# Kernel optimization log

Measured on AMD Instinct MI355X. Metric: run time of the kernel, lower is better.

Reference implementation:

```python
import jax, jax.numpy as jnp
import numpy as np

N = 50000      # nodes
E = 500000     # edges
G = 8          # graphs in batch
H = 64         # latent width (message_passer out_channels)
FIN = 5        # raw node feature dim
MDIM = 3       # mask dim (last col = BC flag)
EF = 3         # edge feature dim
OUT = 4        # output dim
REPEATS = 4    # message passing repeats


def _mlp(h, w1, b1, w2, b2):
    return jnp.dot(jax.nn.relu(jnp.dot(h, w1) + b1), w2) + b2


def _seg_mean(v, idx, n):
    s = jax.ops.segment_sum(v, idx, num_segments=n)
    c = jax.ops.segment_sum(jnp.ones((v.shape[0], 1), v.dtype), idx, num_segments=n)
    return s / jnp.maximum(c, 1.0)


def _lin(k, fi, fo):
    return (jax.random.normal(k, (fi, fo), jnp.float32) / np.sqrt(fi),
            jnp.zeros((fo,), jnp.float32))


def setup_inputs() -> dict:
    key = jax.random.key(0)
    ks = jax.random.split(key, 16)
    x = jax.random.normal(ks[0], (N, FIN), jnp.float32)
    x_mask = jax.random.uniform(ks[1], (N, MDIM), jnp.float32)
    x_mask = x_mask.at[:, -1].set((x_mask[:, -1] > 0.9).astype(jnp.float32))
    edge_index = jax.random.randint(ks[2], (2, E), 0, N, jnp.int32)
    edge_attr = jax.random.normal(ks[3], (E, EF), jnp.float32)
    pos = jax.random.uniform(ks[4], (N, 2), jnp.float32)
    batch = jnp.sort(jax.random.randint(ks[5], (N,), 0, G, jnp.int32))
    enc_w1, enc_b1 = _lin(ks[6], FIN + MDIM, H)
    enc_w2, enc_b2 = _lin(ks[7], H, H)
    msg_w1, msg_b1 = _lin(ks[8], 2 * H + EF, H)
    msg_w2, msg_b2 = _lin(ks[9], H, H)
    upd_w1, upd_b1 = _lin(ks[10], 4 * H, H)
    upd_w2, upd_b2 = _lin(ks[11], H, H)
    dec_w1, dec_b1 = _lin(ks[12], H, H)
    dec_w2, dec_b2 = _lin(ks[13], H, OUT)
    return dict(x=x, x_mask=x_mask, edge_index=edge_index, edge_attr=edge_attr,
                pos=pos, batch=batch,
                enc_w1=enc_w1, enc_b1=enc_b1, enc_w2=enc_w2, enc_b2=enc_b2,
                msg_w1=msg_w1, msg_b1=msg_b1, msg_w2=msg_w2, msg_b2=msg_b2,
                upd_w1=upd_w1, upd_b1=upd_b1, upd_w2=upd_w2, upd_b2=upd_b2,
                dec_w1=dec_w1, dec_b1=dec_b1, dec_w2=dec_w2, dec_b2=dec_b2)


def reference(x, x_mask, edge_index, edge_attr, pos, batch,
              enc_w1, enc_b1, enc_w2, enc_b2,
              msg_w1, msg_b1, msg_w2, msg_b2,
              upd_w1, upd_b1, upd_w2, upd_b2,
              dec_w1, dec_b1, dec_w2, dec_b2):
    # x = concat([x, x_mask]); BC_idxs = x_mask[:, -1]
    bc = x_mask[:, -1:]                                   # [N,1] 0/1 BC flag
    h = _mlp(jnp.concatenate([x, x_mask], axis=1), enc_w1, enc_b1, enc_w2, enc_b2)
    # x_BC = scatter-mean of encoded BC nodes per graph (mask-weighted segment mean)
    bc_sum = jax.ops.segment_sum(h * bc, batch, num_segments=G)
    bc_cnt = jax.ops.segment_sum(bc, batch, num_segments=G)
    x_BC = bc_sum / jnp.maximum(bc_cnt, 1.0)              # [G,H]
    x_graph = _seg_mean(h, batch, G)                      # global_mean_pool [G,H]
    src, dst = edge_index[0], edge_index[1]
    for _ in range(REPEATS):
        # message: MLP over [x_src, x_dst, edge_attr], scatter-mean to dst
        m = _mlp(jnp.concatenate([h[src], h[dst], edge_attr], axis=1),
                 msg_w1, msg_b1, msg_w2, msg_b2)          # [E,H]
        agg = _seg_mean(m, dst, N)                        # [N,H]
        # node update conditioned on global and BC context, residual
        h = h + _mlp(jnp.concatenate([h, agg, x_graph[batch], x_BC[batch]], axis=1),
                     upd_w1, upd_b1, upd_w2, upd_b2)
        x_graph = _seg_mean(h, batch, G)                  # refreshed each repeat
    return _mlp(h, dec_w1, dec_b1, dec_w2, dec_b2)        # [N,OUT]
```

## Files before the change

kernel.cpp:

```cpp
#include <hip/hip_runtime.h>
#include <hip/hip_bf16.h>

#define NN 50000
#define EE 500000
#define GG 8
#define NB 196

#define SCALE_A 65536.0f
#define INV_SCALE_A (1.0f/65536.0f)
#define SCALE_G 16777216.0f
#define INV_SCALE_G (1.0f/16777216.0f)

using short8 = __attribute__((ext_vector_type(8))) short;
using f32x16 = __attribute__((ext_vector_type(16))) float;

__device__ __forceinline__ float4 ld4(const float* p){ return *reinterpret_cast<const float4*>(p); }

__device__ __forceinline__ short f2b(float f){
  union { __hip_bfloat16 b; short s; } u;
  u.b = __float2bfloat16(f);
  return u.s;
}

__global__ __launch_bounds__(256) void k_count(const int* __restrict__ dst, int* __restrict__ cnt){
  int e = blockIdx.x*256 + threadIdx.x;
  if (e < EE) atomicAdd(&cnt[dst[e]], 1);
}

__global__ __launch_bounds__(256) void k_scanA(const int* __restrict__ cnt, int* __restrict__ bsum){
  __shared__ int s[256];
  int t = threadIdx.x;
  int i = blockIdx.x*256 + t;
  s[t] = (i < NN) ? cnt[i] : 0;
  __syncthreads();
  for (int o=128;o>0;o>>=1){ if (t<o) s[t]+=s[t+o]; __syncthreads(); }
  if (t==0) bsum[blockIdx.x] = s[0];
}

__global__ __launch_bounds__(256) void k_scanB(const int* __restrict__ bsum, int* __restrict__ boff){
  __shared__ int s[256];
  int t = threadIdx.x;
  s[t] = (t < NB) ? bsum[t] : 0;
  __syncthreads();
  for (int o=1;o<256;o<<=1){
    int u = (t>=o) ? s[t-o] : 0;
    __syncthreads();
    s[t] += u;
    __syncthreads();
  }
  if (t < NB) boff[t] = (t==0) ? 0 : s[t-1];
}

__global__ __launch_bounds__(256) void k_scanC_prep(const int* __restrict__ cnt, const int* __restrict__ boff,
                                               int* __restrict__ offs,
                                               float* __restrict__ inv, const int* __restrict__ batch,
                                               const float* __restrict__ xm,
                                               float* __restrict__ ncnt, float* __restrict__ bccnt){
  __shared__ int s[256];
  __shared__ float lc[GG], lb[GG];
  int t = threadIdx.x;
  int i = blockIdx.x*256 + t;
  if (t < GG){ lc[t]=0.f; lb[t]=0.f; }
  int v = (i < NN) ? cnt[i] : 0;
  s[t] = v;
  __syncthreads();
  for (int o=1;o<256;o<<=1){
    int u = (t>=o) ? s[t-o] : 0;
    __syncthreads();
    s[t] += u;
    __syncthreads();
  }
  if (i < NN){
    offs[i] = boff[blockIdx.x] + s[t] - v;
    inv[i] = 1.0f / fmaxf((float)v, 1.0f);
    int g = batch[i];
    atomicAdd(&lc[g], 1.0f);
    atomicAdd(&lb[g], xm[i*3+2]);
  }
  __syncthreads();
  if (t < GG){ atomicAdd(&ncnt[t], lc[t]); atomicAdd(&bccnt[t], lb[t]); }
}

__global__ __launch_bounds__(256) void k_prep(const int* __restrict__ cnt, float* __restrict__ inv,
                       const int* __restrict__ batch, const float* __restrict__ xm,
                       float* __restrict__ ncnt, float* __restrict__ bccnt){
  __shared__ float lc[GG], lb[GG];
  int t = threadIdx.x;
  if (t < GG){ lc[t]=0.f; lb[t]=0.f; }
  __syncthreads();
  int i = blockIdx.x*256 + t;
  if (i < NN){
    inv[i] = 1.0f / fmaxf((float)cnt[i], 1.0f);
    int g = batch[i];
    atomicAdd(&lc[g], 1.0f);
    atomicAdd(&lb[g], xm[i*3+2]);
  }
  __syncthreads();
  if (t < GG){ atomicAdd(&ncnt[t], lc[t]); atomicAdd(&bccnt[t], lb[t]); }
}

__global__ __launch_bounds__(256) void k_scat1(const int* __restrict__ dst, int* __restrict__ offs,
                                               int* __restrict__ perm){
  int e = blockIdx.x*256 + threadIdx.x;
  if (e >= EE) return;
  int d = dst[e];
  int pos = atomicAdd(&offs[d], 1);
  perm[pos] = e;
}

__global__ __launch_bounds__(256) void k_scat2(const int* __restrict__ perm,
                                               const int* __restrict__ src, const int* __restrict__ dst,
                                               const float* __restrict__ ea,
                                               int* __restrict__ srcs_s, int* __restrict__ dsts_s,
                                               short* __restrict__ ea16){
  int i = blockIdx.x*256 + threadIdx.x;
  if (i >= EE) return;
  int e = perm[i];
  srcs_s[i] = src[e];
  dsts_s[i] = dst[e];
  int lo = ((int)(unsigned short)f2b(ea[(size_t)e*3+0])) |
           (((int)(unsigned short)f2b(ea[(size_t)e*3+1])) << 16);
  int hi = ((int)(unsigned short)f2b(ea[(size_t)e*3+2]));
  int2 v; v.x = lo; v.y = hi;
  *(int2*)(ea16 + (size_t)i*4) = v;
}

__device__ __forceinline__ void packone(const float* __restrict__ w, int Kreal, int idx, short* __restrict__ out){
  int k = idx >> 6, n = idx & 63;
  float v = (k < Kreal) ? w[k*64 + n] : 0.f;
  int ks = k >> 4, kl = k & 15;
  int lane = (n & 31) + 32*(kl >> 3);
  int e = kl & 7;
  out[(ks*2 + (n>>5))*512 + lane*8 + e] = f2b(v);
}

__global__ __launch_bounds__(256) void k_wpack(
    const float* __restrict__ mw1, const float* __restrict__ mw2,
    const float* __restrict__ uw1, const float* __restrict__ uw2,
    short* __restrict__ mw1p, short* __restrict__ mw2p,
    short* __restrict__ uw1p, short* __restrict__ uw2p){
  int gid = blockIdx.x*256 + threadIdx.x;
  int stride = gridDim.x*256;
  for (int i=gid; i<144*64; i+=stride) packone(mw1, 131, i, mw1p);
  for (int i=gid; i<64*64;  i+=stride) packone(mw2, 64,  i, mw2p);
  for (int i=gid; i<256*64; i+=stride) packone(uw1, 256, i, uw1p);
  for (int i=gid; i<64*64;  i+=stride) packone(uw2, 64,  i, uw2p);
}

__global__ __launch_bounds__(256) void k_enc(
    const float* __restrict__ x, const float* __restrict__ xm,
    const float* __restrict__ w1, const float* __restrict__ b1,
    const float* __restrict__ w2, const float* __restrict__ b2,
    float* __restrict__ h, short* __restrict__ h16){
  __shared__ float w1s[8*64];
  __shared__ float w2s[64*64];
  __shared__ float b1s[64], b2s[64];
  __shared__ float ols[4][64][17];
  int t = threadIdx.x;
  for (int i=t;i<8*64;i+=256) w1s[i]=w1[i];
  for (int i=t;i<64*64;i+=256) w2s[i]=w2[i];
  if (t<64){ b1s[t]=b1[t]; b2s[t]=b2[t]; }
  __syncthreads();
  const int w = t >> 6, lane = t & 63;
  const int base_w = blockIdx.x*256 + w*64;
  const int n = base_w + lane;
  const int nc = (n < NN) ? n : (NN-1);
  float in[8];
  #pragma unroll
  for (int k=0;k<5;k++) in[k] = x[nc*5+k];
  #pragma unroll
  for (int k=0;k<3;k++) in[5+k] = xm[nc*3+k];
  float hid[64];
  #pragma unroll
  for (int o=0;o<64;o++){
    float a = b1s[o];
    #pragma unroll
    for (int k=0;k<8;k++) a += in[k]*w1s[k*64+o];
    hid[o] = fmaxf(a, 0.f);
  }
  for (int c=0;c<4;c++){
    float a[16];
    #pragma unroll
    for (int j=0;j<16;j++) a[j] = b2s[c*16+j];
    for (int k=0;k<64;k++){
      float hv = hid[k];
      #pragma unroll
      for (int j=0;j<16;j++) a[j] += hv * w2s[k*64 + c*16 + j];
    }
    #pragma unroll
    for (int j=0;j<16;j++) ols[w][lane][j] = a[j];
    __syncthreads();
    #pragma unroll
    for (int p=0;p<4;p++){
      int nd = p*16 + (lane>>2);
      int jj = lane & 3;
      int ng = base_w + nd;
      if (ng < NN){
        float4 v = make_float4(ols[w][nd][jj*4+0], ols[w][nd][jj*4+1],
                               ols[w][nd][jj*4+2], ols[w][nd][jj*4+3]);
        *(float4*)(h + (size_t)ng*64 + c*16 + jj*4) = v;
      }
    }
    #pragma unroll
    for (int p=0;p<2;p++){
      int nd = p*32 + (lane>>1);
      int jj = (lane & 1)*8;
      int ng = base_w + nd;
      if (ng < NN){
        short8 s;
        #pragma unroll
        for (int q=0;q<8;q++) s[q] = f2b(ols[w][nd][jj+q]);
        *(short8*)(h16 + (size_t)ng*64 + c*16 + jj) = s;
      }
    }
    __syncthreads();
  }
}

__global__ __launch_bounds__(256) void k_gred(
    const float* __restrict__ h, const int* __restrict__ batch,
    const float* __restrict__ xm,
    unsigned long long* __restrict__ xg_sum, unsigned long long* __restrict__ xbc_sum, int withBC){
  __shared__ float ls[4][GG][64];
  __shared__ float lb[4][GG][64];
  int t = threadIdx.x;
  int d = t & 63, grp = t >> 6;
  for (int g=0; g<GG; g++){ ls[grp][g][d]=0.f; lb[grp][g][d]=0.f; }
  __syncthreads();
  for (int i = blockIdx.x*4 + grp; i < NN; i += gridDim.x*4){
    int g = batch[i];
    float v = h[(size_t)i*64 + d];
    ls[grp][g][d] += v;
    if (withBC) lb[grp][g][d] += v * xm[i*3+2];
  }
  __syncthreads();
  if (t < 64){
    for (int g=0; g<GG; g++){
      float s = ls[0][g][d]+ls[1][g][d]+ls[2][g][d]+ls[3][g][d];
      atomicAdd(&xg_sum[g*64+d], (unsigned long long)(long long)llrintf(s*SCALE_G));
    }
  } else if (withBC && t < 128){
    int dd = t & 63;
    for (int g=0; g<GG; g++){
      float s = lb[0][g][dd]+lb[1][g][dd]+lb[2][g][dd]+lb[3][g][dd];
      atomicAdd(&xbc_sum[g*64+dd], (unsigned long long)(long long)llrintf(s*SCALE_G));
    }
  }
}

__global__ void k_gfin(unsigned long long* __restrict__ xg_sum, const unsigned long long* __restrict__ xbc_sum,
                       const float* __restrict__ ncnt, const float* __restrict__ bccnt,
                       short* __restrict__ xg16, short* __restrict__ xbc16, int withBC){
  int t = threadIdx.x;
  int g = t >> 6;
  float sg = (float)(long long)xg_sum[t] * INV_SCALE_G;
  xg16[t] = f2b(sg / fmaxf(ncnt[g], 1.f));
  xg_sum[t] = 0;
  if (withBC){
    float sb = (float)(long long)xbc_sum[t] * INV_SCALE_G;
    xbc16[t] = f2b(sb / fmaxf(bccnt[g], 1.f));
  }
}

__global__ __launch_bounds__(256) void k_msg_s(
    const short* __restrict__ h16,
    const int* __restrict__ srcs_s, const int* __restrict__ dsts_s,
    const short* __restrict__ ea16,
    const short* __restrict__ w1p, const float* __restrict__ b1,
    const short* __restrict__ w2p, const float* __restrict__ b2,
    int* __restrict__ agg){
  __shared__ int buf[4][2304];
  const int t = threadIdx.x;
  const int w = t >> 6, lane = t & 63;
  const int r = lane & 31, khalf = lane >> 5;
  const int base = blockIdx.x*256 + w*64;

  const int slot = base + lane;
  const int dl = (slot < EE) ? dsts_s[slot] : -1;

  const int eA = base + r, eB = base + 32 + r;
  const bool vA = eA < EE, vB = eB < EE;
  const int sA = vA ? srcs_s[eA] : 0;
  const int sB = vB ? srcs_s[eB] : 0;
  int dA = __shfl(dl, r);        if (dA < 0) dA = 0;
  int dB = __shfl(dl, 32 + r);   if (dB < 0) dB = 0;

  float b1v0 = b1[r], b1v1 = b1[32 + r];
  f32x16 acc00, acc01, acc10, acc11;
  #pragma unroll
  for (int j=0;j<16;j++){ acc00[j]=b1v0; acc01[j]=b1v1; acc10[j]=b1v0; acc11[j]=b1v1; }

  const short8* w1f = (const short8*)w1p;
  #pragma unroll
  for (int ks=0; ks<9; ks++){
    short8 a0, a1;
    if (ks < 8){
      long offA, offB;
      if (ks < 4){
        offA = (long)sA*64 + ks*16 + khalf*8;
        offB = (long)sB*64 + ks*16 + khalf*8;
      } else {
        offA = (long)dA*64 + (ks-4)*16 + khalf*8;
        offB = (long)dB*64 + (ks-4)*16 + khalf*8;
      }
      a0 = *(const short8*)(h16 + offA);
      a1 = *(const short8*)(h16 + offB);
    } else {
      #pragma unroll
      for (int j=0;j<8;j++){ a0[j]=0; a1[j]=0; }
      if (khalf == 0){
        if (vA){
          int2 v = *(const int2*)(ea16 + (size_t)eA*4);
          a0[0]=(short)v.x; a0[1]=(short)(v.x>>16); a0[2]=(short)v.y; a0[3]=(short)(v.y>>16);
        }
        if (vB){
          int2 v = *(const int2*)(ea16 + (size_t)eB*4);
          a1[0]=(short)v.x; a1[1]=(short)(v.x>>16); a1[2]=(short)v.y; a1[3]=(short)(v.y>>16);
        }
      }
    }
    short8 bf0 = w1f[(ks*2+0)*64 + lane];
    short8 bf1 = w1f[(ks*2+1)*64 + lane];
    acc00 = __builtin_amdgcn_mfma_f32_32x32x16_bf16(a0, bf0, acc00, 0, 0, 0);
    acc01 = __builtin_amdgcn_mfma_f32_32x32x16_bf16(a0, bf1, acc01, 0, 0, 0);
    acc10 = __builtin_amdgcn_mfma_f32_32x32x16_bf16(a1, bf0, acc10, 0, 0, 0);
    acc11 = __builtin_amdgcn_mfma_f32_32x32x16_bf16(a1, bf1, acc11, 0, 0, 0);
  }

  short* hw = (short*)&buf[w][0];
  #pragma unroll
  for (int reg=0; reg<16; reg++){
    int row = (reg&3) + 8*(reg>>2) + 4*khalf;
    hw[(row     )*72 + r     ] = f2b(fmaxf(acc00[reg], 0.f));
    hw[(row     )*72 + 32 + r] = f2b(fmaxf(acc01[reg], 0.f));
    hw[(row + 32)*72 + r     ] = f2b(fmaxf(acc10[reg], 0.f));
    hw[(row + 32)*72 + 32 + r] = f2b(fmaxf(acc11[reg], 0.f));
  }

  float b2v0 = b2[r], b2v1 = b2[32 + r];
  f32x16 c00, c01, c10, c11;
  #pragma unroll
  for (int j=0;j<16;j++){ c00[j]=b2v0; c01[j]=b2v1; c10[j]=b2v0; c11[j]=b2v1; }

  const short8* w2f = (const short8*)w2p;
  #pragma unroll
  for (int ks=0; ks<4; ks++){
    short8 a0 = *(const short8*)(hw + (r     )*72 + ks*16 + khalf*8);
    short8 a1 = *(const short8*)(hw + (32 + r)*72 + ks*16 + khalf*8);
    short8 bf0 = w2f[(ks*2+0)*64 + lane];
    short8 bf1 = w2f[(ks*2+1)*64 + lane];
    c00 = __builtin_amdgcn_mfma_f32_32x32x16_bf16(a0, bf0, c00, 0, 0, 0);
    c01 = __builtin_amdgcn_mfma_f32_32x32x16_bf16(a0, bf1, c01, 0, 0, 0);
    c10 = __builtin_amdgcn_mfma_f32_32x32x16_bf16(a1, bf0, c10, 0, 0, 0);
    c11 = __builtin_amdgcn_mfma_f32_32x32x16_bf16(a1, bf1, c11, 0, 0, 0);
  }

  int* mb = &buf[w][0];

  #pragma unroll
  for (int reg=0; reg<16; reg++){
    int row = (reg&3) + 8*(reg>>2) + 4*khalf;
    mb[row*65 + r     ] = __float2int_rn(c00[reg]*SCALE_A);
    mb[row*65 + 32 + r] = __float2int_rn(c01[reg]*SCALE_A);
  }
  {
    int cur = 0;
    while (cur < 32){
      int d = __shfl(dl, cur);
      unsigned long long diff = __ballot(dl != d);
      unsigned low = (unsigned)diff;
      unsigned rest = low & (0xFFFFFFFEu << cur);
      int end = rest ? (__ffs(rest) - 1) : 32;
      if (d >= 0){
        int s = 0;
        for (int rr=cur; rr<end; rr++) s += mb[rr*65 + lane];
        atomicAdd(&agg[(size_t)d*64 + lane], s);
      }
      cur = end;
    }
  }

  #pragma unroll
  for (int reg=0; reg<16; reg++){
    int row = (reg&3) + 8*(reg>>2) + 4*khalf;
    mb[row*65 + r     ] = __float2int_rn(c10[reg]*SCALE_A);
    mb[row*65 + 32 + r] = __float2int_rn(c11[reg]*SCALE_A);
  }
  {
    int cur = 0;
    while (cur < 32){
      int d = __shfl(dl, 32 + cur);
      unsigned long long diff = __ballot(dl != d);
      unsigned hi = (unsigned)(diff >> 32);
      unsigned rest = hi & (0xFFFFFFFEu << cur);
      int end = rest ? (__ffs(rest) - 1) : 32;
      if (d >= 0){
        int s = 0;
        for (int rr=cur; rr<end; rr++) s += mb[rr*65 + lane];
        atomicAdd(&agg[(size_t)d*64 + lane], s);
      }
      cur = end;
    }
  }
}

__global__ __launch_bounds__(256) void k_msg_atomic(
    const short* __restrict__ h16, const int* __restrict__ src, const int* __restrict__ dst,
    const float* __restrict__ ea,
    const short* __restrict__ w1p, const float* __restrict__ b1,
    const short* __restrict__ w2p, const float* __restrict__ b2,
    int* __restrict__ agg){
  __shared__ short hidT[4][64*72];
  const int t = threadIdx.x;
  const int w = t >> 6, lane = t & 63;
  const int r = lane & 31, khalf = lane >> 5;
  const int base = blockIdx.x*256 + w*64;
  const int eA = base + r, eB = base + 32 + r;
  const bool vA = eA < EE, vB = eB < EE;
  const int sA = vA ? src[eA] : 0, dA_ = vA ? dst[eA] : 0;
  const int sB = vB ? src[eB] : 0, dB_ = vB ? dst[eB] : 0;

  float b1v0 = b1[r], b1v1 = b1[32 + r];
  f32x16 acc00, acc01, acc10, acc11;
  #pragma unroll
  for (int j=0;j<16;j++){ acc00[j]=b1v0; acc01[j]=b1v1; acc10[j]=b1v0; acc11[j]=b1v1; }

  const short8* w1f = (const short8*)w1p;
  #pragma unroll
  for (int ks=0; ks<9; ks++){
    short8 a0, a1;
    if (ks < 8){
      long offA, offB;
      if (ks < 4){
        offA = (long)sA*64 + ks*16 + khalf*8;
        offB = (long)sB*64 + ks*16 + khalf*8;
      } else {
        offA = (long)dA_*64 + (ks-4)*16 + khalf*8;
        offB = (long)dB_*64 + (ks-4)*16 + khalf*8;
      }
      a0 = *(const short8*)(h16 + offA);
      a1 = *(const short8*)(h16 + offB);
    } else {
      #pragma unroll
      for (int j=0;j<8;j++){ a0[j]=0; a1[j]=0; }
      if (khalf == 0){
        if (vA){ a0[0]=f2b(ea[3*eA]); a0[1]=f2b(ea[3*eA+1]); a0[2]=f2b(ea[3*eA+2]); }
        if (vB){ a1[0]=f2b(ea[3*eB]); a1[1]=f2b(ea[3*eB+1]); a1[2]=f2b(ea[3*eB+2]); }
      }
    }
    short8 bf0 = w1f[(ks*2+0)*64 + lane];
    short8 bf1 = w1f[(ks*2+1)*64 + lane];
    acc00 = __builtin_amdgcn_mfma_f32_32x32x16_bf16(a0, bf0, acc00, 0, 0, 0);
    acc01 = __builtin_amdgcn_mfma_f32_32x32x16_bf16(a0, bf1, acc01, 0, 0, 0);
    acc10 = __builtin_amdgcn_mfma_f32_32x32x16_bf16(a1, bf0, acc10, 0, 0, 0);
    acc11 = __builtin_amdgcn_mfma_f32_32x32x16_bf16(a1, bf1, acc11, 0, 0, 0);
  }

  short* hw = &hidT[w][0];
  #pragma unroll
  for (int reg=0; reg<16; reg++){
    int row = (reg&3) + 8*(reg>>2) + 4*khalf;
    hw[(row     )*72 + r     ] = f2b(fmaxf(acc00[reg], 0.f));
    hw[(row     )*72 + 32 + r] = f2b(fmaxf(acc01[reg], 0.f));
    hw[(row + 32)*72 + r     ] = f2b(fmaxf(acc10[reg], 0.f));
    hw[(row + 32)*72 + 32 + r] = f2b(fmaxf(acc11[reg], 0.f));
  }

  float b2v0 = b2[r], b2v1 = b2[32 + r];
  f32x16 c00, c01, c10, c11;
  #pragma unroll
  for (int j=0;j<16;j++){ c00[j]=b2v0; c01[j]=b2v1; c10[j]=b2v0; c11[j]=b2v1; }

  const short8* w2f = (const short8*)w2p;
  #pragma unroll
  for (int ks=0; ks<4; ks++){
    short8 a0 = *(const short8*)(hw + (r     )*72 + ks*16 + khalf*8);
    short8 a1 = *(const short8*)(hw + (32 + r)*72 + ks*16 + khalf*8);
    short8 bf0 = w2f[(ks*2+0)*64 + lane];
    short8 bf1 = w2f[(ks*2+1)*64 + lane];
    c00 = __builtin_amdgcn_mfma_f32_32x32x16_bf16(a0, bf0, c00, 0, 0, 0);
    c01 = __builtin_amdgcn_mfma_f32_32x32x16_bf16(a0, bf1, c01, 0, 0, 0);
    c10 = __builtin_amdgcn_mfma_f32_32x32x16_bf16(a1, bf0, c10, 0, 0, 0);
    c11 = __builtin_amdgcn_mfma_f32_32x32x16_bf16(a1, bf1, c11, 0, 0, 0);
  }

  #pragma unroll
  for (int reg=0; reg<16; reg++){
    int row = (reg&3) + 8*(reg>>2) + 4*khalf;
    int e0r = base + row;
    int e1r = base + 32 + row;
    int d0 = __shfl(dA_, row);
    int d1 = __shfl(dB_, row);
    if (e0r < EE){
      atomicAdd(&agg[(size_t)d0*64 + r     ], __float2int_rn(c00[reg]*SCALE_A));
      atomicAdd(&agg[(size_t)d0*64 + 32 + r], __float2int_rn(c01[reg]*SCALE_A));
    }
    if (e1r < EE){
      atomicAdd(&agg[(size_t)d1*64 + r     ], __float2int_rn(c10[reg]*SCALE_A));
      atomicAdd(&agg[(size_t)d1*64 + 32 + r], __float2int_rn(c11[reg]*SCALE_A));
    }
  }
}

__global__ __launch_bounds__(256) void k_upd(
    float* __restrict__ h32, short* __restrict__ h16,
    int* __restrict__ agg, const float* __restrict__ inv,
    const int* __restrict__ batch,
    const short* __restrict__ xg16, const short* __restrict__ xbc16,
    const short* __restrict__ w1p, const float* __restrict__ b1,
    const short* __restrict__ w2p, const float* __restrict__ b2,
    unsigned long long* __restrict__ xg_sum, int withG){
  __shared__ short hidT[4][32*72];
  __shared__ unsigned long long gs[GG*64];
  const int t = threadIdx.x;
  for (int i=t; i<GG*64; i+=256) gs[i]=0;
  __syncthreads();

  const int w = t >> 6, lane = t & 63;
  const int r = lane & 31, khalf = lane >> 5;
  const int n0 = blockIdx.x*128 + w*32;
  const int n = n0 + r;
  const int nc = (n < NN) ? n : (NN-1);
  const int g = batch[nc];
  const float sc = inv[nc] * INV_SCALE_A;

  float b1v0 = b1[r], b1v1 = b1[32 + r];
  f32x16 a0acc, a1acc;
  #pragma unroll
  for (int j=0;j<16;j++){ a0acc[j]=b1v0; a1acc[j]=b1v1; }

  const short8* w1f = (const short8*)w1p;
  #pragma unroll
  for (int ks=0; ks<16; ks++){
    short8 a;
    int so = (ks & 3)*16 + khalf*8;
    if (ks < 4){
      a = *(const short8*)(h16 + (long)nc*64 + so);
    } else if (ks < 8){
      int4 i0 = *(const int4*)(agg + (long)nc*64 + so);
      int4 i1 = *(const int4*)(agg + (long)nc*64 + so + 4);
      if (n < NN){
        *(int4*)(agg + (long)nc*64 + so)     = make_int4(0,0,0,0);
        *(int4*)(agg + (long)nc*64 + so + 4) = make_int4(0,0,0,0);
      }
      a[0]=f2b((float)i0.x*sc); a[1]=f2b((float)i0.y*sc); a[2]=f2b((float)i0.z*sc); a[3]=f2b((float)i0.w*sc);
      a[4]=f2b((float)i1.x*sc); a[5]=f2b((float)i1.y*sc); a[6]=f2b((float)i1.z*sc); a[7]=f2b((float)i1.w*sc);
    } else if (ks < 12){
      a = *(const short8*)(xg16 + g*64 + so);
    } else {
      a = *(const short8*)(xbc16 + g*64 + so);
    }
    short8 bf0 = w1f[(ks*2+0)*64 + lane];
    short8 bf1 = w1f[(ks*2+1)*64 + lane];
    a0acc = __builtin_amdgcn_mfma_f32_32x32x16_bf16(a, bf0, a0acc, 0, 0, 0);
    a1acc = __builtin_amdgcn_mfma_f32_32x32x16_bf16(a, bf1, a1acc, 0, 0, 0);
  }

  short* hw = &hidT[w][0];
  #pragma unroll
  for (int reg=0; reg<16; reg++){
    int row = (reg&3) + 8*(reg>>2) + 4*khalf;
    hw[row*72 + r     ] = f2b(fmaxf(a0acc[reg], 0.f));
    hw[row*72 + 32 + r] = f2b(fmaxf(a1acc[reg], 0.f));
  }

  float b2v0 = b2[r], b2v1 = b2[32 + r];
  f32x16 c0, c1;
  #pragma unroll
  for (int j=0;j<16;j++){ c0[j]=b2v0; c1[j]=b2v1; }

  const short8* w2f = (const short8*)w2p;
  #pragma unroll
  for (int ks=0; ks<4; ks++){
    short8 a = *(const short8*)(hw + r*72 + ks*16 + khalf*8);
    short8 bf0 = w2f[(ks*2+0)*64 + lane];
    short8 bf1 = w2f[(ks*2+1)*64 + lane];
    c0 = __builtin_amdgcn_mfma_f32_32x32x16_bf16(a, bf0, c0, 0, 0, 0);
    c1 = __builtin_amdgcn_mfma_f32_32x32x16_bf16(a, bf1, c1, 0, 0, 0);
  }

  const bool doG = (withG != 0);
  const int g0 = __shfl(g, 0), g31 = __shfl(g, 31);
  const bool uni = (g0 == g31);
  long long s0 = 0, s1 = 0;
  #pragma unroll
  for (int reg=0; reg<16; reg++){
    int row = (reg&3) + 8*(reg>>2) + 4*khalf;
    int gg = __shfl(g, row);
    int nn = n0 + row;
    if (nn < NN){
      size_t i0 = (size_t)nn*64 + r;
      float v0 = h32[i0] + c0[reg];
      float v1 = h32[i0+32] + c1[reg];
      h32[i0] = v0;    h16[i0] = f2b(v0);
      h32[i0+32] = v1; h16[i0+32] = f2b(v1);
      if (doG){
        long long q0 = llrintf(v0*SCALE_G), q1 = llrintf(v1*SCALE_G);
        if (uni){ s0 += q0; s1 += q1; }
        else {
          atomicAdd(&gs[gg*64 + r     ], (unsigned long long)q0);
          atomicAdd(&gs[gg*64 + 32 + r], (unsigned long long)q1);
        }
      }
    }
  }
  if (doG && uni && (s0|s1)){
    atomicAdd(&gs[g0*64 + r     ], (unsigned long long)s0);
    atomicAdd(&gs[g0*64 + 32 + r], (unsigned long long)s1);
  }
  __syncthreads();
  if (doG){
    for (int i=t; i<GG*64; i+=256){
      unsigned long long v = gs[i];
      if (v) atomicAdd(&xg_sum[i], v);
    }
  }
}

__global__ __launch_bounds__(256) void k_dec(
    const float* __restrict__ h,
    const float* __restrict__ w1, const float* __restrict__ b1,
    const float* __restrict__ w2, const float* __restrict__ b2,
    float* __restrict__ out){
  __shared__ float w1s[64*64];
  __shared__ float w2s[64*4];
  __shared__ float b1s[64], b2s[4];
  int t=threadIdx.x;
  for (int i=t;i<64*64;i+=256) w1s[i]=w1[i];
  for (int i=t;i<256;i+=256) w2s[i]=w2[i];
  if (t<64) b1s[t]=b1[t];
  if (t<4) b2s[t]=b2[t];
  __syncthreads();
  int n = blockIdx.x*256+t;
  if (n>=NN) return;
  float xr[64];
  #pragma unroll
  for (int k=0;k<64;k++) xr[k] = h[(size_t)n*64+k];
  float a0=b2s[0],a1=b2s[1],a2=b2s[2],a3=b2s[3];
  for (int o=0;o<64;o++){
    float a=b1s[o];
    #pragma unroll
    for (int k=0;k<64;k++) a += xr[k]*w1s[k*64+o];
    a = fmaxf(a,0.f);
    a0 += a*w2s[o*4+0]; a1 += a*w2s[o*4+1]; a2 += a*w2s[o*4+2]; a3 += a*w2s[o*4+3];
  }
  out[(size_t)n*4+0]=a0; out[(size_t)n*4+1]=a1; out[(size_t)n*4+2]=a2; out[(size_t)n*4+3]=a3;
}

extern "C" void kernel_launch(void* const* d_in, const int* in_sizes, int n_in,
                              void* d_out, int out_size, void* d_ws, size_t ws_size,
                              hipStream_t stream){
  const float* x   = (const float*)d_in[0];
  const float* xm  = (const float*)d_in[1];
  const int*   ei  = (const int*)d_in[2];
  const float* ea  = (const float*)d_in[3];
  const int* batch = (const int*)d_in[5];
  const float* enc_w1=(const float*)d_in[6],  *enc_b1=(const float*)d_in[7];
  const float* enc_w2=(const float*)d_in[8],  *enc_b2=(const float*)d_in[9];
  const float* msg_w1=(const float*)d_in[10], *msg_b1=(const float*)d_in[11];
  const float* msg_w2=(const float*)d_in[12], *msg_b2=(const float*)d_in[13];
  const float* upd_w1=(const float*)d_in[14], *upd_b1=(const float*)d_in[15];
  const float* upd_w2=(const float*)d_in[16], *upd_b2=(const float*)d_in[17];
  const float* dec_w1=(const float*)d_in[18], *dec_b1=(const float*)d_in[19];
  const float* dec_w2=(const float*)d_in[20], *dec_b2=(const float*)d_in[21];
  const int* srcp = ei;
  const int* dstp = ei + EE;

  char* ws = (char*)d_ws;
  float* h32     = (float*)(ws + 0);
  int*   agg     = (int*)  (ws + 12800000);
  short* h16     = (short*)(ws + 25600000);
  float* inv     = (float*)(ws + 32000000);
  int*   cnt     = (int*)  (ws + 32200000);
  unsigned long long* xg_sum  = (unsigned long long*)(ws + 32400000);
  unsigned long long* xbc_sum = (unsigned long long*)(ws + 32404096);
  float* ncnt    = (float*)(ws + 32408192);
  float* bccnt   = (float*)(ws + 32408224);
  short* xg16    = (short*)(ws + 32408256);
  short* xbc16   = (short*)(ws + 32409280);
  short* mw1p    = (short*)(ws + 32410304);
  short* mw2p    = (short*)(ws + 32428736);
  short* uw1p    = (short*)(ws + 32436928);
  short* uw2p    = (short*)(ws + 32469696);
  int*   offs    = (int*)  (ws + 32477888);
  int*   srcs_s  = (int*)  (ws + 32677888);
  int*   dsts_s  = (int*)  (ws + 34678784);
  short* ea16s   = (short*)(ws + 36679680);
  int*   bsum    = (int*)  (ws + 40681472);
  int*   boff    = (int*)  (ws + 40682272);
  int*   perm    = (int*)  (ws + 40683072);
  const size_t WS_NEED_SORT = 42683968;
  const int useSort = (ws_size >= WS_NEED_SORT) ? 1 : 0;

  hipMemsetAsync(ws + 32200000, 0, 208256, stream);
  hipMemsetAsync(agg, 0, 12800000, stream);
  k_wpack<<<34, 256, 0, stream>>>(msg_w1, msg_w2, upd_w1, upd_w2, mw1p, mw2p, uw1p, uw2p);
  k_count<<<(EE+255)/256, 256, 0, stream>>>(dstp, cnt);
  if (useSort){
    k_scanA<<<NB, 256, 0, stream>>>(cnt, bsum);
    k_scanB<<<1, 256, 0, stream>>>(bsum, boff);
    k_scanC_prep<<<NB, 256, 0, stream>>>(cnt, boff, offs, inv, batch, xm, ncnt, bccnt);
    k_scat1<<<(EE+255)/256, 256, 0, stream>>>(dstp, offs, perm);
    k_scat2<<<(EE+255)/256, 256, 0, stream>>>(perm, srcp, dstp, ea, srcs_s, dsts_s, ea16s);
  } else {
    k_prep<<<(NN+255)/256, 256, 0, stream>>>(cnt, inv, batch, xm, ncnt, bccnt);
  }
  k_enc<<<(NN+255)/256, 256, 0, stream>>>(x, xm, enc_w1, enc_b1, enc_w2, enc_b2, h32, h16);
  k_gred<<<512, 256, 0, stream>>>(h32, batch, xm, xg_sum, xbc_sum, 1);
  k_gfin<<<1, 512, 0, stream>>>(xg_sum, xbc_sum, ncnt, bccnt, xg16, xbc16, 1);

  for (int rp=0; rp<4; rp++){
    if (useSort){
      k_msg_s<<<(EE+255)/256, 256, 0, stream>>>(h16, srcs_s, dsts_s, ea16s, mw1p, msg_b1, mw2p, msg_b2, agg);
    } else {
      k_msg_atomic<<<(EE+255)/256, 256, 0, stream>>>(h16, srcp, dstp, ea, mw1p, msg_b1, mw2p, msg_b2, agg);
    }
    int withG = (rp < 3) ? 1 : 0;
    k_upd<<<(NN+127)/128, 256, 0, stream>>>(h32, h16, agg, inv, batch, xg16, xbc16, uw1p, upd_b1, uw2p, upd_b2, xg_sum, withG);
    if (withG) k_gfin<<<1, 512, 0, stream>>>(xg_sum, xbc_sum, ncnt, bccnt, xg16, xbc16, 0);
  }
  k_dec<<<(NN+255)/256, 256, 0, stream>>>(h32, dec_w1, dec_b1, dec_w2, dec_b2, (float*)d_out);
}
```

Baseline: 412.2 us.

## Halve edges per wave in sorted message kernel and vectorize decoder loads

The sorted-edge message kernel now gives each wave 32 edges instead of 64. It keeps two accumulator tiles instead of four, preloads all nine A fragments up front, and halves the shared-memory buffer by switching it to short. The segmented scatter reduction now runs in two 16-row passes and clamps each segment end to the pass boundary. The aim is lower register and LDS pressure for higher occupancy and better latency hiding of the gathers, at the cost of twice as many blocks, reloading the weight fragments per wave, and possibly more atomics at segment boundaries. The decoder also switches its row loads to float4.

```diff
diff --git a/kernel.cpp b/kernel.cpp
--- a/kernel.cpp
+++ b/kernel.cpp
@@ -269,134 +269,92 @@
     const short* __restrict__ w1p, const float* __restrict__ b1,
     const short* __restrict__ w2p, const float* __restrict__ b2,
     int* __restrict__ agg){
-  __shared__ int buf[4][2304];
+  __shared__ short hid[4][2304];
   const int t = threadIdx.x;
   const int w = t >> 6, lane = t & 63;
   const int r = lane & 31, khalf = lane >> 5;
-  const int base = blockIdx.x*256 + w*64;
-
-  const int slot = base + lane;
-  const int dl = (slot < EE) ? dsts_s[slot] : -1;
-
-  const int eA = base + r, eB = base + 32 + r;
-  const bool vA = eA < EE, vB = eB < EE;
-  const int sA = vA ? srcs_s[eA] : 0;
-  const int sB = vB ? srcs_s[eB] : 0;
-  int dA = __shfl(dl, r);        if (dA < 0) dA = 0;
-  int dB = __shfl(dl, 32 + r);   if (dB < 0) dB = 0;
+  const int base = blockIdx.x*128 + w*32;
+  const int e = base + r;
+  const bool ve = e < EE;
+  const int dl = ve ? dsts_s[e] : -1;
+  const int sA = ve ? srcs_s[e] : 0;
+  const int dA = (dl < 0) ? 0 : dl;
+
+  short8 a[9];
+  #pragma unroll
+  for (int ks=0;ks<4;ks++) a[ks]   = *(const short8*)(h16 + (long)sA*64 + ks*16 + khalf*8);
+  #pragma unroll
+  for (int ks=0;ks<4;ks++) a[4+ks] = *(const short8*)(h16 + (long)dA*64 + ks*16 + khalf*8);
+  {
+    short8 z;
+    #pragma unroll
+    for (int j=0;j<8;j++) z[j]=0;
+    if (khalf == 0 && ve){
+      int2 v = *(const int2*)(ea16 + (size_t)e*4);
+      z[0]=(short)v.x; z[1]=(short)(v.x>>16); z[2]=(short)v.y; z[3]=(short)(v.y>>16);
+    }
+    a[8] = z;
+  }
 
   float b1v0 = b1[r], b1v1 = b1[32 + r];
-  f32x16 acc00, acc01, acc10, acc11;
-  #pragma unroll
-  for (int j=0;j<16;j++){ acc00[j]=b1v0; acc01[j]=b1v1; acc10[j]=b1v0; acc11[j]=b1v1; }
+  f32x16 acc0, acc1;
+  #pragma unroll
+  for (int j=0;j<16;j++){ acc0[j]=b1v0; acc1[j]=b1v1; }
 
   const short8* w1f = (const short8*)w1p;
   #pragma unroll
   for (int ks=0; ks<9; ks++){
-    short8 a0, a1;
-    if (ks < 8){
-      long offA, offB;
-      if (ks < 4){
-        offA = (long)sA*64 + ks*16 + khalf*8;
-        offB = (long)sB*64 + ks*16 + khalf*8;
-      } else {
-        offA = (long)dA*64 + (ks-4)*16 + khalf*8;
-        offB = (long)dB*64 + (ks-4)*16 + khalf*8;
-      }
-      a0 = *(const short8*)(h16 + offA);
-      a1 = *(const short8*)(h16 + offB);
-    } else {
-      #pragma unroll
-      for (int j=0;j<8;j++){ a0[j]=0; a1[j]=0; }
-      if (khalf == 0){
-        if (vA){
-          int2 v = *(const int2*)(ea16 + (size_t)eA*4);
-          a0[0]=(short)v.x; a0[1]=(short)(v.x>>16); a0[2]=(short)v.y; a0[3]=(short)(v.y>>16);
-        }
-        if (vB){
-          int2 v = *(const int2*)(ea16 + (size_t)eB*4);
-          a1[0]=(short)v.x; a1[1]=(short)(v.x>>16); a1[2]=(short)v.y; a1[3]=(short)(v.y>>16);
-        }
-      }
-    }
     short8 bf0 = w1f[(ks*2+0)*64 + lane];
     short8 bf1 = w1f[(ks*2+1)*64 + lane];
-    acc00 = __builtin_amdgcn_mfma_f32_32x32x16_bf16(a0, bf0, acc00, 0, 0, 0);
-    acc01 = __builtin_amdgcn_mfma_f32_32x32x16_bf16(a0, bf1, acc01, 0, 0, 0);
-    acc10 = __builtin_amdgcn_mfma_f32_32x32x16_bf16(a1, bf0, acc10, 0, 0, 0);
-    acc11 = __builtin_amdgcn_mfma_f32_32x32x16_bf16(a1, bf1, acc11, 0, 0, 0);
-  }
-
-  short* hw = (short*)&buf[w][0];
+    acc0 = __builtin_amdgcn_mfma_f32_32x32x16_bf16(a[ks], bf0, acc0, 0, 0, 0);
+    acc1 = __builtin_amdgcn_mfma_f32_32x32x16_bf16(a[ks], bf1, acc1, 0, 0, 0);
+  }
+
+  short* hw = &hid[w][0];
   #pragma unroll
   for (int reg=0; reg<16; reg++){
     int row = (reg&3) + 8*(reg>>2) + 4*khalf;
-    hw[(row     )*72 + r     ] = f2b(fmaxf(acc00[reg], 0.f));
-    hw[(row     )*72 + 32 + r] = f2b(fmaxf(acc01[reg], 0.f));
-    hw[(row + 32)*72 + r     ] = f2b(fmaxf(acc10[reg], 0.f));
-    hw[(row + 32)*72 + 32 + r] = f2b(fmaxf(acc11[reg], 0.f));
+    hw[row*72 + r     ] = f2b(fmaxf(acc0[reg], 0.f));
+    hw[row*72 + 32 + r] = f2b(fmaxf(acc1[reg], 0.f));
   }
 
   float b2v0 = b2[r], b2v1 = b2[32 + r];
-  f32x16 c00, c01, c10, c11;
-  #pragma unroll
-  for (int j=0;j<16;j++){ c00[j]=b2v0; c01[j]=b2v1; c10[j]=b2v0; c11[j]=b2v1; }
+  f32x16 c0, c1;
+  #pragma unroll
+  for (int j=0;j<16;j++){ c0[j]=b2v0; c1[j]=b2v1; }
 
   const short8* w2f = (const short8*)w2p;
   #pragma unroll
   for (int ks=0; ks<4; ks++){
-    short8 a0 = *(const short8*)(hw + (r     )*72 + ks*16 + khalf*8);
-    short8 a1 = *(const short8*)(hw + (32 + r)*72 + ks*16 + khalf*8);
+    short8 aa = *(const short8*)(hw + r*72 + ks*16 + khalf*8);
     short8 bf0 = w2f[(ks*2+0)*64 + lane];
     short8 bf1 = w2f[(ks*2+1)*64 + lane];
-    c00 = __builtin_amdgcn_mfma_f32_32x32x16_bf16(a0, bf0, c00, 0, 0, 0);
-    c01 = __builtin_amdgcn_mfma_f32_32x32x16_bf16(a0, bf1, c01, 0, 0, 0);
-    c10 = __builtin_amdgcn_mfma_f32_32x32x16_bf16(a1, bf0, c10, 0, 0, 0);
-    c11 = __builtin_amdgcn_mfma_f32_32x32x16_bf16(a1, bf1, c11, 0, 0, 0);
-  }
-
-  int* mb = &buf[w][0];
-
-  #pragma unroll
-  for (int reg=0; reg<16; reg++){
-    int row = (reg&3) + 8*(reg>>2) + 4*khalf;
-    mb[row*65 + r     ] = __float2int_rn(c00[reg]*SCALE_A);
-    mb[row*65 + 32 + r] = __float2int_rn(c01[reg]*SCALE_A);
-  }
-  {
-    int cur = 0;
-    while (cur < 32){
+    c0 = __builtin_amdgcn_mfma_f32_32x32x16_bf16(aa, bf0, c0, 0, 0, 0);
+    c1 = __builtin_amdgcn_mfma_f32_32x32x16_bf16(aa, bf1, c1, 0, 0, 0);
+  }
+
+  int* mb = (int*)&hid[w][0];
+  #pragma unroll
+  for (int pass=0; pass<2; pass++){
+    const int w0 = pass*16;
+    #pragma unroll
+    for (int q=0; q<8; q++){
+      int reg = pass*8 + q;
+      int row = (reg&3) + 8*(reg>>2) + 4*khalf;
+      mb[(row - w0)*65 + r     ] = __float2int_rn(c0[reg]*SCALE_A);
+      mb[(row - w0)*65 + 32 + r] = __float2int_rn(c1[reg]*SCALE_A);
+    }
+    int cur = w0;
+    while (cur < w0 + 16){
       int d = __shfl(dl, cur);
       unsigned long long diff = __ballot(dl != d);
       unsigned low = (unsigned)diff;
       unsigned rest = low & (0xFFFFFFFEu << cur);
-      int end = rest ? (__ffs(rest) - 1) : 32;
+      int nd = rest ? (__ffs(rest) - 1) : 32;
+      int end = (nd < w0 + 16) ? nd : (w0 + 16);
       if (d >= 0){
         int s = 0;
-        for (int rr=cur; rr<end; rr++) s += mb[rr*65 + lane];
-        atomicAdd(&agg[(size_t)d*64 + lane], s);
-      }
-      cur = end;
-    }
-  }
-
-  #pragma unroll
-  for (int reg=0; reg<16; reg++){
-    int row = (reg&3) + 8*(reg>>2) + 4*khalf;
-    mb[row*65 + r     ] = __float2int_rn(c10[reg]*SCALE_A);
-    mb[row*65 + 32 + r] = __float2int_rn(c11[reg]*SCALE_A);
-  }
-  {
-    int cur = 0;
-    while (cur < 32){
-      int d = __shfl(dl, 32 + cur);
-      unsigned long long diff = __ballot(dl != d);
-      unsigned hi = (unsigned)(diff >> 32);
-      unsigned rest = hi & (0xFFFFFFFEu << cur);
-      int end = rest ? (__ffs(rest) - 1) : 32;
-      if (d >= 0){
-        int s = 0;
-        for (int rr=cur; rr<end; rr++) s += mb[rr*65 + lane];
+        for (int rr=cur; rr<end; rr++) s += mb[(rr - w0)*65 + lane];
         atomicAdd(&agg[(size_t)d*64 + lane], s);
       }
       cur = end;
@@ -635,7 +593,10 @@
   if (n>=NN) return;
   float xr[64];
   #pragma unroll
-  for (int k=0;k<64;k++) xr[k] = h[(size_t)n*64+k];
+  for (int k=0;k<16;k++){
+    float4 v = ld4(h + (size_t)n*64 + k*4);
+    xr[k*4+0]=v.x; xr[k*4+1]=v.y; xr[k*4+2]=v.z; xr[k*4+3]=v.w;
+  }
   float a0=b2s[0],a1=b2s[1],a2=b2s[2],a3=b2s[3];
   for (int o=0;o<64;o++){
     float a=b1s[o];
@@ -711,7 +672,7 @@
 
   for (int rp=0; rp<4; rp++){
     if (useSort){
-      k_msg_s<<<(EE+255)/256, 256, 0, stream>>>(h16, srcs_s, dsts_s, ea16s, mw1p, msg_b1, mw2p, msg_b2, agg);
+      k_msg_s<<<(EE+127)/128, 256, 0, stream>>>(h16, srcs_s, dsts_s, ea16s, mw1p, msg_b1, mw2p, msg_b2, agg);
     } else {
       k_msg_atomic<<<(EE+255)/256, 256, 0, stream>>>(h16, srcp, dstp, ea, mw1p, msg_b1, mw2p, msg_b2, agg);
     }
```

Measured after the change: 444.3 us. +7.8%, slower.
